# Kernel optimization log

Hardware: AMD Instinct MI355X
Metric: run time of the kernel (lower is better)

Reference implementation:

```python
import jax, jax.numpy as jnp
import numpy as np


def setup_inputs() -> dict:
    key = jax.random.key(0)
    kq, kk, kv = jax.random.split(key, 3)
    B, S, D = 16, 2048, 128
    q = jax.random.normal(kq, (B, S, D), dtype=jnp.float32)
    k = jax.random.normal(kk, (B, S, D), dtype=jnp.float32)
    v = jax.random.normal(kv, (B, S, D), dtype=jnp.float32)
    return {"q": q, "k": k, "v": v}


def reference(q, k, v):
    # q: (B, Sq, Dk), k: (B, Skv, Dk), v: (B, Skv, Dv)
    d_k = k.shape[-1]
    scale = 1.0 / jnp.sqrt(jnp.asarray(d_k, dtype=q.dtype))
    scores = jnp.einsum("bqd,bkd->bqk", q, k) * scale  # (B, Sq, Skv)
    # causal mask: strictly-upper-triangular positions set to -inf (mask=True in init)
    Sq = q.shape[-2]
    causal = jnp.triu(jnp.ones((Sq, Sq), dtype=bool), k=1)
    scores = jnp.where(causal, -jnp.inf, scores)
    attn = jax.nn.softmax(scores, axis=-1)
    return jnp.einsum("bqk,bkd->bqd", attn, v)
```

## Files before the change

kernel.cpp:

```cpp
#include <hip/hip_runtime.h>
#include <hip/hip_bf16.h>

typedef __bf16 bf16;
typedef bf16 bf16x8 __attribute__((ext_vector_type(8)));
typedef bf16 bf16x4 __attribute__((ext_vector_type(4)));
typedef float f32x4 __attribute__((ext_vector_type(4)));

#define DHEAD 128
#define SCL2 0.1275500811965365f
#define NINF (-__builtin_inff())

__device__ __forceinline__ unsigned pk2(float a, float b) {
  bf16 x = (bf16)a, y = (bf16)b;
  unsigned short ux = __builtin_bit_cast(unsigned short, x);
  unsigned short uy = __builtin_bit_cast(unsigned short, y);
  return ((unsigned)uy << 16) | (unsigned)ux;
}

#define ACC_FLOATS (1024 * 64 * 128)
#define ML_OFF ACC_FLOATS
#define WS_NEED ((size_t)(ACC_FLOATS + 1024 * 64 * 2) * 4)

#define ACC4_FLOATS (2048 * 64 * 128)
#define ML4_OFF ACC4_FLOATS
#define WS_NEED4 ((size_t)(ACC4_FLOATS + 2048 * 64 * 2) * 4)

__global__ __launch_bounds__(256) void fa_split4(
    const float* __restrict__ Q, const float* __restrict__ K,
    const float* __restrict__ V, float* __restrict__ ws, int S)
{
  const int bid  = blockIdx.x;
  const int half = bid >> 9;
  const int w    = bid & 511;
  const int qt   = 31 - (w >> 4);
  const int b    = w & 15;
  const int blk  = bid;

  const int NT = 2 * (qt + 1);
  const int t0 = (half * NT) >> 2;
  const int t1 = ((half + 1) * NT) >> 2;

  const int tid  = threadIdx.x;
  const int wave = tid >> 6;
  const int lane = tid & 63;
  const int lr   = lane & 15;
  const int lg   = lane >> 4;

  __shared__ bf16 Ks[32][136];
  __shared__ bf16 Vt[DHEAD][40];
  __shared__ bf16 Ps[4][16][40];

  const size_t bo = (size_t)b * S * DHEAD;
  const float* Qb = Q + bo + (size_t)qt * 64 * DHEAD;
  const float* Kb = K + bo;
  const float* Vb = V + bo;
  const int wrow0 = qt * 64 + wave * 16;

  const int j   = tid & 31;
  const int prw = tid >> 5;
  const int d4  = j << 2;
  const int Gw  = (j >> 1) & 3;

  bf16x8 qf[4];
  {
    const float* qr = Qb + (size_t)(wave * 16 + lr) * DHEAD;
    #pragma unroll
    for (int c = 0; c < 4; ++c) {
      const float4 u0 = *reinterpret_cast<const float4*>(qr + c * 32 + lg * 8);
      const float4 u1 = *reinterpret_cast<const float4*>(qr + c * 32 + lg * 8 + 4);
      bf16x8 f;
      f[0] = (bf16)(u0.x * SCL2); f[1] = (bf16)(u0.y * SCL2);
      f[2] = (bf16)(u0.z * SCL2); f[3] = (bf16)(u0.w * SCL2);
      f[4] = (bf16)(u1.x * SCL2); f[5] = (bf16)(u1.y * SCL2);
      f[6] = (bf16)(u1.z * SCL2); f[7] = (bf16)(u1.w * SCL2);
      qf[c] = f;
    }
  }

  f32x4 oacc[8];
  #pragma unroll
  for (int ii = 0; ii < 8; ++ii) oacc[ii] = (f32x4){0.f, 0.f, 0.f, 0.f};
  float m = NINF, l = 0.f;

  float4 kA[2], kB[2], vA[2], vB[2];
  auto load_tile = [&](int kc) {
    #pragma unroll
    for (int ps = 0; ps < 2; ++ps) {
      const int kv = kc + 2 * (prw + 8 * ps);
      const float* kp = Kb + (size_t)kv * DHEAD + d4;
      const float* vp = Vb + (size_t)kv * DHEAD + d4;
      kA[ps] = *reinterpret_cast<const float4*>(kp);
      kB[ps] = *reinterpret_cast<const float4*>(kp + DHEAD);
      vA[ps] = *reinterpret_cast<const float4*>(vp);
      vB[ps] = *reinterpret_cast<const float4*>(vp + DHEAD);
    }
  };
  auto write_tile = [&]() {
    #pragma unroll
    for (int ps = 0; ps < 2; ++ps) {
      const int kvp = prw + 8 * ps;
      bf16x4 ka, kb;
      ka[0] = (bf16)kA[ps].x; ka[1] = (bf16)kA[ps].y;
      ka[2] = (bf16)kA[ps].z; ka[3] = (bf16)kA[ps].w;
      kb[0] = (bf16)kB[ps].x; kb[1] = (bf16)kB[ps].y;
      kb[2] = (bf16)kB[ps].z; kb[3] = (bf16)kB[ps].w;
      *reinterpret_cast<bf16x4*>(&Ks[2 * kvp][d4])     = ka;
      *reinterpret_cast<bf16x4*>(&Ks[2 * kvp + 1][d4]) = kb;
      const int pS = kvp ^ (Gw << 2);
      const float* fa = &vA[ps].x;
      const float* fb = &vB[ps].x;
      #pragma unroll
      for (int c = 0; c < 4; ++c) {
        *reinterpret_cast<unsigned*>(&Vt[d4 + c][2 * pS]) = pk2(fa[c], fb[c]);
      }
    }
  };

  if (t0 < t1) load_tile(t0 * 32);

  for (int t = t0; t < t1; ++t) {
    __syncthreads();
    write_tile();
    if (t + 1 < t1) load_tile((t + 1) * 32);
    __syncthreads();

    const int kc = t * 32;
    if (kc <= wrow0 + 15) {
      f32x4 s0 = {0.f, 0.f, 0.f, 0.f}, s1 = {0.f, 0.f, 0.f, 0.f};
      __builtin_amdgcn_s_setprio(1);
      #pragma unroll
      for (int c = 0; c < 4; ++c) {
        const bf16x8 kf0 = *reinterpret_cast<const bf16x8*>(&Ks[lr][c * 32 + lg * 8]);
        const bf16x8 kf1 = *reinterpret_cast<const bf16x8*>(&Ks[16 + lr][c * 32 + lg * 8]);
        s0 = __builtin_amdgcn_mfma_f32_16x16x32_bf16(kf0, qf[c], s0, 0, 0, 0);
        s1 = __builtin_amdgcn_mfma_f32_16x16x32_bf16(kf1, qf[c], s1, 0, 0, 0);
      }
      __builtin_amdgcn_s_setprio(0);

      const int qg = wrow0 + lr;
      float x0[4], x1[4];
      if (kc + 31 > wrow0) {
        #pragma unroll
        for (int rr = 0; rr < 4; ++rr) {
          x0[rr] = (kc + 4 * lg + rr      > qg) ? NINF : s0[rr];
          x1[rr] = (kc + 16 + 4 * lg + rr > qg) ? NINF : s1[rr];
        }
      } else {
        #pragma unroll
        for (int rr = 0; rr < 4; ++rr) { x0[rr] = s0[rr]; x1[rr] = s1[rr]; }
      }
      float tm = NINF;
      #pragma unroll
      for (int rr = 0; rr < 4; ++rr) tm = fmaxf(tm, fmaxf(x0[rr], x1[rr]));
      tm = fmaxf(tm, __shfl_xor(tm, 16));
      tm = fmaxf(tm, __shfl_xor(tm, 32));

      if (!__all(tm <= m + 8.0f)) {
        const float mn = fmaxf(m, tm);
        const float al = __builtin_exp2f(m - mn);
        m = mn; l *= al;
        #pragma unroll
        for (int rr = 0; rr < 4; ++rr) {
          const float ar = __shfl(al, 4 * lg + rr);
          #pragma unroll
          for (int ds = 0; ds < 8; ++ds) oacc[ds][rr] *= ar;
        }
      }

      float p0[4], p1[4];
      float ts = 0.f;
      #pragma unroll
      for (int rr = 0; rr < 4; ++rr) {
        p0[rr] = __builtin_exp2f(x0[rr] - m);
        p1[rr] = __builtin_exp2f(x1[rr] - m);
        ts += p0[rr] + p1[rr];
      }
      ts += __shfl_xor(ts, 16);
      ts += __shfl_xor(ts, 32);
      l += ts;

      *reinterpret_cast<unsigned*>(&Ps[wave][lr][4 * lg])          = pk2(p0[0], p0[1]);
      *reinterpret_cast<unsigned*>(&Ps[wave][lr][4 * lg + 2])      = pk2(p0[2], p0[3]);
      *reinterpret_cast<unsigned*>(&Ps[wave][lr][16 + 4 * lg])     = pk2(p1[0], p1[1]);
      *reinterpret_cast<unsigned*>(&Ps[wave][lr][16 + 4 * lg + 2]) = pk2(p1[2], p1[3]);

      const bf16x8 pf = *reinterpret_cast<const bf16x8*>(&Ps[wave][lr][lg * 8]);
      __builtin_amdgcn_s_setprio(1);
      #pragma unroll
      for (int ds = 0; ds < 8; ++ds) {
        const int G = (2 * ds + (lr >> 3)) & 3;
        const bf16x8 vf = *reinterpret_cast<const bf16x8*>(&Vt[ds * 16 + lr][8 * (lg ^ G)]);
        oacc[ds] = __builtin_amdgcn_mfma_f32_16x16x32_bf16(pf, vf, oacc[ds], 0, 0, 0);
      }
      __builtin_amdgcn_s_setprio(0);
    }
  }

  float* aw = ws + (size_t)blk * 8192 + (size_t)(wave * 16) * 128;
  #pragma unroll
  for (int rr = 0; rr < 4; ++rr) {
    #pragma unroll
    for (int ds = 0; ds < 8; ++ds) {
      aw[(4 * lg + rr) * 128 + ds * 16 + lr] = oacc[ds][rr];
    }
  }
  if (lg == 0) {
    float* mlp = ws + ML4_OFF + (size_t)(blk * 64 + wave * 16 + lr) * 2;
    mlp[0] = m;
    mlp[1] = l;
  }
}

__global__ __launch_bounds__(256) void fa_merge4(
    const float* __restrict__ ws, float* __restrict__ O, int S)
{
  const int blk2 = blockIdx.x;
  const int b  = blk2 >> 5;
  const int qt = blk2 & 31;
  const int tid = threadIdx.x;
  const int row = tid >> 2;
  const int c0  = (tid & 3) * 32;

  const int w = (31 - qt) * 16 + b;
  float mi[4], li[4];
  float mm = NINF;
  #pragma unroll
  for (int i = 0; i < 4; ++i) {
    const float* ml = ws + ML4_OFF + (size_t)((i * 512 + w) * 64 + row) * 2;
    mi[i] = ml[0]; li[i] = ml[1];
    mm = fmaxf(mm, mi[i]);
  }
  float a[4], den = 0.f;
  #pragma unroll
  for (int i = 0; i < 4; ++i) { a[i] = __builtin_exp2f(mi[i] - mm); den += a[i] * li[i]; }
  const float inv = 1.0f / den;

  float* out = O + ((size_t)b * S + qt * 64 + row) * DHEAD + c0;
  #pragma unroll
  for (int qd = 0; qd < 8; ++qd) {
    float4 acc = {0.f, 0.f, 0.f, 0.f};
    #pragma unroll
    for (int i = 0; i < 4; ++i) {
      const float* wp = ws + (size_t)(i * 512 + w) * 8192 + (size_t)row * 128 + c0;
      const float4 u = *reinterpret_cast<const float4*>(wp + qd * 4);
      acc.x += a[i] * u.x; acc.y += a[i] * u.y;
      acc.z += a[i] * u.z; acc.w += a[i] * u.w;
    }
    float4 o;
    o.x = acc.x * inv; o.y = acc.y * inv; o.z = acc.z * inv; o.w = acc.w * inv;
    *reinterpret_cast<float4*>(out + qd * 4) = o;
  }
}

__global__ __launch_bounds__(256) void fa_split(
    const float* __restrict__ Q, const float* __restrict__ K,
    const float* __restrict__ V, float* __restrict__ ws, int S)
{
  const int bid  = blockIdx.x;
  const int r    = bid >> 8;
  const int i    = bid & 255;
  const int b    = i & 15;
  const int idx  = i >> 4;
  const int qt   = (r < 2) ? (31 - idx) : idx;
  const int half = r & 1;
  const int blk  = bid;

  const int t0 = half * (qt + 1);
  const int t1 = t0 + (qt + 1);

  const int tid  = threadIdx.x;
  const int wave = tid >> 6;
  const int lane = tid & 63;
  const int lr   = lane & 15;
  const int lg   = lane >> 4;

  __shared__ bf16 Ks[2][32][136];
  __shared__ bf16 Vt[2][DHEAD][40];
  __shared__ bf16 Ps[4][16][40];

  const size_t bo = (size_t)b * S * DHEAD;
  const float* Qb = Q + bo + (size_t)qt * 64 * DHEAD;
  const float* Kb = K + bo;
  const float* Vb = V + bo;
  const int wrow0 = qt * 64 + wave * 16;

  const int j   = tid & 31;
  const int prw = tid >> 5;
  const int d4  = j << 2;
  const int Gw  = (j >> 1) & 3;

  bf16x8 qf[4];
  {
    const float* qr = Qb + (size_t)(wave * 16 + lr) * DHEAD;
    #pragma unroll
    for (int c = 0; c < 4; ++c) {
      const float4 u0 = *reinterpret_cast<const float4*>(qr + c * 32 + lg * 8);
      const float4 u1 = *reinterpret_cast<const float4*>(qr + c * 32 + lg * 8 + 4);
      bf16x8 f;
      f[0] = (bf16)u0.x; f[1] = (bf16)u0.y; f[2] = (bf16)u0.z; f[3] = (bf16)u0.w;
      f[4] = (bf16)u1.x; f[5] = (bf16)u1.y; f[6] = (bf16)u1.z; f[7] = (bf16)u1.w;
      qf[c] = f;
    }
  }

  f32x4 oacc[8];
  #pragma unroll
  for (int ii = 0; ii < 8; ++ii) oacc[ii] = (f32x4){0.f, 0.f, 0.f, 0.f};
  float m = NINF, l = 0.f;

  float4 kA[2], kB[2], vA[2], vB[2];
  auto load_tile = [&](int kc) {
    #pragma unroll
    for (int ps = 0; ps < 2; ++ps) {
      const int kv = kc + 2 * (prw + 8 * ps);
      const float* kp = Kb + (size_t)kv * DHEAD + d4;
      const float* vp = Vb + (size_t)kv * DHEAD + d4;
      kA[ps] = *reinterpret_cast<const float4*>(kp);
      kB[ps] = *reinterpret_cast<const float4*>(kp + DHEAD);
      vA[ps] = *reinterpret_cast<const float4*>(vp);
      vB[ps] = *reinterpret_cast<const float4*>(vp + DHEAD);
    }
  };
  auto write_tile = [&](int buf) {
    #pragma unroll
    for (int ps = 0; ps < 2; ++ps) {
      const int kvp = prw + 8 * ps;
      bf16x4 ka, kb;
      ka[0] = (bf16)kA[ps].x; ka[1] = (bf16)kA[ps].y;
      ka[2] = (bf16)kA[ps].z; ka[3] = (bf16)kA[ps].w;
      kb[0] = (bf16)kB[ps].x; kb[1] = (bf16)kB[ps].y;
      kb[2] = (bf16)kB[ps].z; kb[3] = (bf16)kB[ps].w;
      *reinterpret_cast<bf16x4*>(&Ks[buf][2 * kvp][d4])     = ka;
      *reinterpret_cast<bf16x4*>(&Ks[buf][2 * kvp + 1][d4]) = kb;
      const int pS = kvp ^ (Gw << 2);
      const float* fa = &vA[ps].x;
      const float* fb = &vB[ps].x;
      #pragma unroll
      for (int c = 0; c < 4; ++c) {
        *reinterpret_cast<unsigned*>(&Vt[buf][d4 + c][2 * pS]) = pk2(fa[c], fb[c]);
      }
    }
  };

  load_tile(t0 * 32);
  write_tile(0);
  if (t0 + 1 < t1) load_tile((t0 + 1) * 32);

  int cur = 0;
  for (int t = t0; t < t1; ++t) {
    __syncthreads();
    if (t + 1 < t1) write_tile(cur ^ 1);
    if (t + 2 < t1) load_tile((t + 2) * 32);

    const int kc = t * 32;
    if (kc <= wrow0 + 15) {
      f32x4 s0 = {0.f, 0.f, 0.f, 0.f}, s1 = {0.f, 0.f, 0.f, 0.f};
      __builtin_amdgcn_s_setprio(1);
      #pragma unroll
      for (int c = 0; c < 4; ++c) {
        const bf16x8 kf0 = *reinterpret_cast<const bf16x8*>(&Ks[cur][lr][c * 32 + lg * 8]);
        const bf16x8 kf1 = *reinterpret_cast<const bf16x8*>(&Ks[cur][16 + lr][c * 32 + lg * 8]);
        s0 = __builtin_amdgcn_mfma_f32_16x16x32_bf16(kf0, qf[c], s0, 0, 0, 0);
        s1 = __builtin_amdgcn_mfma_f32_16x16x32_bf16(kf1, qf[c], s1, 0, 0, 0);
      }
      __builtin_amdgcn_s_setprio(0);

      const int qg = wrow0 + lr;
      float x0[4], x1[4];
      if (kc + 31 > wrow0) {
        #pragma unroll
        for (int rr = 0; rr < 4; ++rr) {
          x0[rr] = (kc + 4 * lg + rr      > qg) ? NINF : s0[rr] * SCL2;
          x1[rr] = (kc + 16 + 4 * lg + rr > qg) ? NINF : s1[rr] * SCL2;
        }
      } else {
        #pragma unroll
        for (int rr = 0; rr < 4; ++rr) { x0[rr] = s0[rr] * SCL2; x1[rr] = s1[rr] * SCL2; }
      }
      float tm = NINF;
      #pragma unroll
      for (int rr = 0; rr < 4; ++rr) tm = fmaxf(tm, fmaxf(x0[rr], x1[rr]));
      tm = fmaxf(tm, __shfl_xor(tm, 16));
      tm = fmaxf(tm, __shfl_xor(tm, 32));

      if (!__all(tm <= m + 8.0f)) {
        const float mn = fmaxf(m, tm);
        const float al = __builtin_exp2f(m - mn);
        m = mn; l *= al;
        #pragma unroll
        for (int rr = 0; rr < 4; ++rr) {
          const float ar = __shfl(al, 4 * lg + rr);
          #pragma unroll
          for (int ds = 0; ds < 8; ++ds) oacc[ds][rr] *= ar;
        }
      }

      float p0[4], p1[4];
      float ts = 0.f;
      #pragma unroll
      for (int rr = 0; rr < 4; ++rr) {
        p0[rr] = __builtin_exp2f(x0[rr] - m);
        p1[rr] = __builtin_exp2f(x1[rr] - m);
        ts += p0[rr] + p1[rr];
      }
      ts += __shfl_xor(ts, 16);
      ts += __shfl_xor(ts, 32);
      l += ts;

      *reinterpret_cast<unsigned*>(&Ps[wave][lr][4 * lg])          = pk2(p0[0], p0[1]);
      *reinterpret_cast<unsigned*>(&Ps[wave][lr][4 * lg + 2])      = pk2(p0[2], p0[3]);
      *reinterpret_cast<unsigned*>(&Ps[wave][lr][16 + 4 * lg])     = pk2(p1[0], p1[1]);
      *reinterpret_cast<unsigned*>(&Ps[wave][lr][16 + 4 * lg + 2]) = pk2(p1[2], p1[3]);

      const bf16x8 pf = *reinterpret_cast<const bf16x8*>(&Ps[wave][lr][lg * 8]);
      __builtin_amdgcn_s_setprio(1);
      #pragma unroll
      for (int ds = 0; ds < 8; ++ds) {
        const int G = (2 * ds + (lr >> 3)) & 3;
        const bf16x8 vf = *reinterpret_cast<const bf16x8*>(&Vt[cur][ds * 16 + lr][8 * (lg ^ G)]);
        oacc[ds] = __builtin_amdgcn_mfma_f32_16x16x32_bf16(pf, vf, oacc[ds], 0, 0, 0);
      }
      __builtin_amdgcn_s_setprio(0);
    }
    cur ^= 1;
  }

  float* aw = ws + (size_t)blk * 8192 + (size_t)(wave * 16) * 128;
  #pragma unroll
  for (int rr = 0; rr < 4; ++rr) {
    #pragma unroll
    for (int ds = 0; ds < 8; ++ds) {
      aw[(4 * lg + rr) * 128 + ds * 16 + lr] = oacc[ds][rr];
    }
  }
  if (lg == 0) {
    float* mlp = ws + ML_OFF + (size_t)(blk * 64 + wave * 16 + lr) * 2;
    mlp[0] = m;
    mlp[1] = l;
  }
}

__global__ __launch_bounds__(256) void fa_merge(
    const float* __restrict__ ws, float* __restrict__ O, int S)
{
  const int blk2 = blockIdx.x;
  const int b  = blk2 >> 5;
  const int qt = blk2 & 31;
  const int tid = threadIdx.x;
  const int row = tid >> 2;
  const int c0  = (tid & 3) * 32;

  const int idx  = (qt >= 16) ? (31 - qt) : qt;
  const int base = (qt >= 16) ? 0 : 512;
  const int blk0 = base + (idx << 4) + b;
  const int blk1 = blk0 + 256;

  const float* ml0 = ws + ML_OFF + (size_t)(blk0 * 64 + row) * 2;
  const float* ml1 = ws + ML_OFF + (size_t)(blk1 * 64 + row) * 2;
  const float m0 = ml0[0], l0 = ml0[1];
  const float m1 = ml1[0], l1 = ml1[1];
  const float mm = fmaxf(m0, m1);
  const float a0 = __builtin_exp2f(m0 - mm);
  const float a1 = __builtin_exp2f(m1 - mm);
  const float inv = 1.0f / (a0 * l0 + a1 * l1);

  const float* w0 = ws + (size_t)blk0 * 8192 + (size_t)row * 128 + c0;
  const float* w1 = ws + (size_t)blk1 * 8192 + (size_t)row * 128 + c0;
  float* out = O + ((size_t)b * S + qt * 64 + row) * DHEAD + c0;

  #pragma unroll
  for (int qd = 0; qd < 8; ++qd) {
    const float4 u0 = *reinterpret_cast<const float4*>(w0 + qd * 4);
    const float4 u1 = *reinterpret_cast<const float4*>(w1 + qd * 4);
    float4 o;
    o.x = (a0 * u0.x + a1 * u1.x) * inv;
    o.y = (a0 * u0.y + a1 * u1.y) * inv;
    o.z = (a0 * u0.z + a1 * u1.z) * inv;
    o.w = (a0 * u0.w + a1 * u1.w) * inv;
    *reinterpret_cast<float4*>(out + qd * 4) = o;
  }
}

__global__ __launch_bounds__(256) void fa_fwd(
    const float* __restrict__ Q, const float* __restrict__ K,
    const float* __restrict__ V, float* __restrict__ O, int S)
{
  const int bid = blockIdx.x;
  const int prb = bid & 255;
  const int hb  = bid >> 8;
  const int b   = prb & 15;
  const int jj  = prb >> 4;
  const int qt  = hb ? jj : (31 - jj);

  const int tid  = threadIdx.x;
  const int wave = tid >> 6;
  const int lane = tid & 63;
  const int lr   = lane & 15;
  const int lg   = lane >> 4;

  __shared__ bf16 Ks[2][32][136];
  __shared__ bf16 Vt[2][DHEAD][40];
  __shared__ bf16 Ps[4][16][40];

  const size_t bo = (size_t)b * S * DHEAD;
  const float* Qb = Q + bo + (size_t)qt * 64 * DHEAD;
  const float* Kb = K + bo;
  const float* Vb = V + bo;
  const int wrow0 = qt * 64 + wave * 16;

  const int j   = tid & 31;
  const int prw = tid >> 5;
  const int d4  = j << 2;
  const int Gw  = (j >> 1) & 3;

  bf16x8 qf[4];
  {
    const float* qr = Qb + (size_t)(wave * 16 + lr) * DHEAD;
    #pragma unroll
    for (int c = 0; c < 4; ++c) {
      const float4 u0 = *reinterpret_cast<const float4*>(qr + c * 32 + lg * 8);
      const float4 u1 = *reinterpret_cast<const float4*>(qr + c * 32 + lg * 8 + 4);
      bf16x8 f;
      f[0] = (bf16)u0.x; f[1] = (bf16)u0.y; f[2] = (bf16)u0.z; f[3] = (bf16)u0.w;
      f[4] = (bf16)u1.x; f[5] = (bf16)u1.y; f[6] = (bf16)u1.z; f[7] = (bf16)u1.w;
      qf[c] = f;
    }
  }

  f32x4 oacc[8];
  #pragma unroll
  for (int ii = 0; ii < 8; ++ii) oacc[ii] = (f32x4){0.f, 0.f, 0.f, 0.f};
  float m = NINF, l = 0.f;

  const int nt = 2 * (qt + 1);
  float4 kA[2], kB[2], vA[2], vB[2];

  auto load_tile = [&](int kc) {
    #pragma unroll
    for (int ps = 0; ps < 2; ++ps) {
      const int kv = kc + 2 * (prw + 8 * ps);
      const float* kp = Kb + (size_t)kv * DHEAD + d4;
      const float* vp = Vb + (size_t)kv * DHEAD + d4;
      kA[ps] = *reinterpret_cast<const float4*>(kp);
      kB[ps] = *reinterpret_cast<const float4*>(kp + DHEAD);
      vA[ps] = *reinterpret_cast<const float4*>(vp);
      vB[ps] = *reinterpret_cast<const float4*>(vp + DHEAD);
    }
  };
  auto write_tile = [&](int buf) {
    #pragma unroll
    for (int ps = 0; ps < 2; ++ps) {
      const int kvp = prw + 8 * ps;
      bf16x4 ka, kb;
      ka[0] = (bf16)kA[ps].x; ka[1] = (bf16)kA[ps].y;
      ka[2] = (bf16)kA[ps].z; ka[3] = (bf16)kA[ps].w;
      kb[0] = (bf16)kB[ps].x; kb[1] = (bf16)kB[ps].y;
      kb[2] = (bf16)kB[ps].z; kb[3] = (bf16)kB[ps].w;
      *reinterpret_cast<bf16x4*>(&Ks[buf][2 * kvp][d4])     = ka;
      *reinterpret_cast<bf16x4*>(&Ks[buf][2 * kvp + 1][d4]) = kb;
      const int pS = kvp ^ (Gw << 2);
      const float* fa = &vA[ps].x;
      const float* fb = &vB[ps].x;
      #pragma unroll
      for (int c = 0; c < 4; ++c) {
        *reinterpret_cast<unsigned*>(&Vt[buf][d4 + c][2 * pS]) = pk2(fa[c], fb[c]);
      }
    }
  };

  load_tile(0);
  write_tile(0);
  if (nt > 1) load_tile(32);

  int cur = 0;
  for (int t = 0; t < nt; ++t) {
    __syncthreads();
    if (t + 1 < nt) write_tile(cur ^ 1);
    if (t + 2 < nt) load_tile((t + 2) * 32);

    const int kc = t * 32;
    if (kc <= wrow0 + 15) {
      f32x4 s0 = {0.f, 0.f, 0.f, 0.f}, s1 = {0.f, 0.f, 0.f, 0.f};
      __builtin_amdgcn_s_setprio(1);
      #pragma unroll
      for (int c = 0; c < 4; ++c) {
        const bf16x8 kf0 = *reinterpret_cast<const bf16x8*>(&Ks[cur][lr][c * 32 + lg * 8]);
        const bf16x8 kf1 = *reinterpret_cast<const bf16x8*>(&Ks[cur][16 + lr][c * 32 + lg * 8]);
        s0 = __builtin_amdgcn_mfma_f32_16x16x32_bf16(kf0, qf[c], s0, 0, 0, 0);
        s1 = __builtin_amdgcn_mfma_f32_16x16x32_bf16(kf1, qf[c], s1, 0, 0, 0);
      }
      __builtin_amdgcn_s_setprio(0);

      const int qg = wrow0 + lr;
      float x0[4], x1[4];
      if (kc + 31 > wrow0) {
        #pragma unroll
        for (int rr = 0; rr < 4; ++rr) {
          x0[rr] = (kc + 4 * lg + rr      > qg) ? NINF : s0[rr] * SCL2;
          x1[rr] = (kc + 16 + 4 * lg + rr > qg) ? NINF : s1[rr] * SCL2;
        }
      } else {
        #pragma unroll
        for (int rr = 0; rr < 4; ++rr) { x0[rr] = s0[rr] * SCL2; x1[rr] = s1[rr] * SCL2; }
      }
      float tm = NINF;
      #pragma unroll
      for (int rr = 0; rr < 4; ++rr) tm = fmaxf(tm, fmaxf(x0[rr], x1[rr]));
      tm = fmaxf(tm, __shfl_xor(tm, 16));
      tm = fmaxf(tm, __shfl_xor(tm, 32));

      if (!__all(tm <= m + 8.0f)) {
        const float mn = fmaxf(m, tm);
        const float al = __builtin_exp2f(m - mn);
        m = mn; l *= al;
        #pragma unroll
        for (int rr = 0; rr < 4; ++rr) {
          const float ar = __shfl(al, 4 * lg + rr);
          #pragma unroll
          for (int ds = 0; ds < 8; ++ds) oacc[ds][rr] *= ar;
        }
      }

      float p0[4], p1[4];
      float ts = 0.f;
      #pragma unroll
      for (int rr = 0; rr < 4; ++rr) {
        p0[rr] = __builtin_exp2f(x0[rr] - m);
        p1[rr] = __builtin_exp2f(x1[rr] - m);
        ts += p0[rr] + p1[rr];
      }
      ts += __shfl_xor(ts, 16);
      ts += __shfl_xor(ts, 32);
      l += ts;

      *reinterpret_cast<unsigned*>(&Ps[wave][lr][4 * lg])          = pk2(p0[0], p0[1]);
      *reinterpret_cast<unsigned*>(&Ps[wave][lr][4 * lg + 2])      = pk2(p0[2], p0[3]);
      *reinterpret_cast<unsigned*>(&Ps[wave][lr][16 + 4 * lg])     = pk2(p1[0], p1[1]);
      *reinterpret_cast<unsigned*>(&Ps[wave][lr][16 + 4 * lg + 2]) = pk2(p1[2], p1[3]);

      const bf16x8 pf = *reinterpret_cast<const bf16x8*>(&Ps[wave][lr][lg * 8]);
      __builtin_amdgcn_s_setprio(1);
      #pragma unroll
      for (int ds = 0; ds < 8; ++ds) {
        const int G = (2 * ds + (lr >> 3)) & 3;
        const bf16x8 vf = *reinterpret_cast<const bf16x8*>(&Vt[cur][ds * 16 + lr][8 * (lg ^ G)]);
        oacc[ds] = __builtin_amdgcn_mfma_f32_16x16x32_bf16(pf, vf, oacc[ds], 0, 0, 0);
      }
      __builtin_amdgcn_s_setprio(0);
    }
    cur ^= 1;
  }

  const float linv = 1.0f / l;
  float* Ob = O + bo + (size_t)(qt * 64 + wave * 16) * DHEAD;
  #pragma unroll
  for (int rr = 0; rr < 4; ++rr) {
    const float ir = __shfl(linv, 4 * lg + rr);
    #pragma unroll
    for (int ds = 0; ds < 8; ++ds) {
      Ob[(size_t)(4 * lg + rr) * DHEAD + ds * 16 + lr] = oacc[ds][rr] * ir;
    }
  }
}

extern "C" void kernel_launch(void* const* d_in, const int* in_sizes, int n_in,
                              void* d_out, int out_size, void* d_ws, size_t ws_size,
                              hipStream_t stream) {
  const float* q = (const float*)d_in[0];
  const float* k = (const float*)d_in[1];
  const float* v = (const float*)d_in[2];
  float* o = (float*)d_out;

  const int B = 16;
  const int S = in_sizes[0] / (B * DHEAD);

  if (ws_size >= WS_NEED4 && S == 2048) {
    float* ws = (float*)d_ws;
    fa_split4<<<dim3(2048), dim3(256), 0, stream>>>(q, k, v, ws, S);
    fa_merge4<<<dim3(512), dim3(256), 0, stream>>>(ws, o, S);
  } else if (ws_size >= WS_NEED && S == 2048) {
    float* ws = (float*)d_ws;
    fa_split<<<dim3(1024), dim3(256), 0, stream>>>(q, k, v, ws, S);
    fa_merge<<<dim3(512), dim3(256), 0, stream>>>(ws, o, S);
  } else {
    fa_fwd<<<dim3(512), dim3(256), 0, stream>>>(q, k, v, o, S);
  }
}
```

Baseline: 185.4 us.

## Pre-convert K/V to bf16 with transposed V and read MFMA operands from global

Adds a prep kernel that converts K to bf16 and V to a bf16 transposed layout in workspace. The new split kernel then reads MFMA operands straight from global/L2 instead of staging them through LDS with double buffering and barriers. Q is prescaled before the bf16 cast, and the block order is remapped for L2 locality, with a matching merge kernel. This removes repeated fp32 K/V loads and conversions per query tile and drops the syncthreads, but adds an extra launch and global traffic, and relies on cache hits for the uncoalesced-ish direct loads. The fallback paths are kept and the old two-way split path is removed.

Measured after the change: 257.6 us. 1.39x slower.

```diff
diff --git a/kernel.cpp b/kernel.cpp
--- a/kernel.cpp
+++ b/kernel.cpp
@@ -17,13 +17,239 @@
   return ((unsigned)uy << 16) | (unsigned)ux;
 }
 
-#define ACC_FLOATS (1024 * 64 * 128)
-#define ML_OFF ACC_FLOATS
-#define WS_NEED ((size_t)(ACC_FLOATS + 1024 * 64 * 2) * 4)
-
 #define ACC4_FLOATS (2048 * 64 * 128)
 #define ML4_OFF ACC4_FLOATS
-#define WS_NEED4 ((size_t)(ACC4_FLOATS + 2048 * 64 * 2) * 4)
+#define ACC_ML_FLOATS (ACC4_FLOATS + 2048 * 64 * 2)
+#define WS_NEED4 ((size_t)ACC_ML_FLOATS * 4)
+#define KV_BASE_BYTES ((size_t)ACC_ML_FLOATS * 4)
+#define KV_BYTES ((size_t)16 * 2048 * 128 * 2)
+#define WS_DIRECT (KV_BASE_BYTES + 2 * KV_BYTES)
+
+__global__ __launch_bounds__(256) void fa_prep(
+    const float* __restrict__ K, const float* __restrict__ V,
+    bf16* __restrict__ Kb, bf16* __restrict__ Vt, int S)
+{
+  const int b   = blockIdx.x >> 5;
+  const int kv0 = (blockIdx.x & 31) * 64;
+  const int tid = threadIdx.x;
+
+  __shared__ float Vl[64][132];
+
+  const float* Kbase = K + ((size_t)b * S + kv0) * DHEAD;
+  const float* Vbase = V + ((size_t)b * S + kv0) * DHEAD;
+  bf16* Kout = Kb + ((size_t)b * S + kv0) * DHEAD;
+
+  #pragma unroll
+  for (int i = 0; i < 8; ++i) {
+    const int flat = i * 256 + tid;
+    const int row  = flat >> 5;
+    const int c4   = (flat & 31) << 2;
+    const float4 kv4 = *reinterpret_cast<const float4*>(Kbase + (size_t)row * DHEAD + c4);
+    bf16x4 kp;
+    kp[0] = (bf16)kv4.x; kp[1] = (bf16)kv4.y; kp[2] = (bf16)kv4.z; kp[3] = (bf16)kv4.w;
+    *reinterpret_cast<bf16x4*>(Kout + (size_t)row * DHEAD + c4) = kp;
+    const float4 vv4 = *reinterpret_cast<const float4*>(Vbase + (size_t)row * DHEAD + c4);
+    Vl[row][c4 + 0] = vv4.x; Vl[row][c4 + 1] = vv4.y;
+    Vl[row][c4 + 2] = vv4.z; Vl[row][c4 + 3] = vv4.w;
+  }
+  __syncthreads();
+
+  #pragma unroll
+  for (int i = 0; i < 8; ++i) {
+    const int flat = i * 256 + tid;
+    const int d    = flat >> 4;
+    const int kvg  = (flat & 15) << 2;
+    bf16x4 vp;
+    vp[0] = (bf16)Vl[kvg + 0][d]; vp[1] = (bf16)Vl[kvg + 1][d];
+    vp[2] = (bf16)Vl[kvg + 2][d]; vp[3] = (bf16)Vl[kvg + 3][d];
+    *reinterpret_cast<bf16x4*>(Vt + ((size_t)b * DHEAD + d) * S + kv0 + kvg) = vp;
+  }
+}
+
+__global__ __launch_bounds__(256) void fa_direct(
+    const float* __restrict__ Q, const bf16* __restrict__ Kb,
+    const bf16* __restrict__ Vt, float* __restrict__ ws, int S)
+{
+  const int bid  = blockIdx.x;
+  const int blo  = bid & 7;
+  const int rest = bid >> 3;
+  const int half = rest & 3;
+  const int bhi  = (rest >> 2) & 1;
+  const int qt   = 31 - (rest >> 3);
+  const int b    = blo | (bhi << 3);
+  const int blk  = bid;
+
+  const int NT = 2 * (qt + 1);
+  const int t0 = (half * NT) >> 2;
+  const int t1 = ((half + 1) * NT) >> 2;
+
+  const int tid  = threadIdx.x;
+  const int wave = tid >> 6;
+  const int lane = tid & 63;
+  const int lr   = lane & 15;
+  const int lg   = lane >> 4;
+
+  __shared__ bf16 Ps[4][16][40];
+
+  const float* Qb = Q + ((size_t)b * S + qt * 64) * DHEAD;
+  const bf16* Kbb = Kb + (size_t)b * S * DHEAD;
+  const bf16* Vtb = Vt + (size_t)b * DHEAD * S;
+  const int wrow0 = qt * 64 + wave * 16;
+
+  bf16x8 qf[4];
+  {
+    const float* qr = Qb + (size_t)(wave * 16 + lr) * DHEAD;
+    #pragma unroll
+    for (int c = 0; c < 4; ++c) {
+      const float4 u0 = *reinterpret_cast<const float4*>(qr + c * 32 + lg * 8);
+      const float4 u1 = *reinterpret_cast<const float4*>(qr + c * 32 + lg * 8 + 4);
+      bf16x8 f;
+      f[0] = (bf16)(u0.x * SCL2); f[1] = (bf16)(u0.y * SCL2);
+      f[2] = (bf16)(u0.z * SCL2); f[3] = (bf16)(u0.w * SCL2);
+      f[4] = (bf16)(u1.x * SCL2); f[5] = (bf16)(u1.y * SCL2);
+      f[6] = (bf16)(u1.z * SCL2); f[7] = (bf16)(u1.w * SCL2);
+      qf[c] = f;
+    }
+  }
+
+  f32x4 oacc[8];
+  #pragma unroll
+  for (int ii = 0; ii < 8; ++ii) oacc[ii] = (f32x4){0.f, 0.f, 0.f, 0.f};
+  float m = NINF, l = 0.f;
+
+  for (int t = t0; t < t1; ++t) {
+    const int kc = t * 32;
+    if (kc > wrow0 + 15) continue;
+
+    const bf16* krow0 = Kbb + (size_t)(kc + lr) * DHEAD + lg * 8;
+    const bf16* krow1 = krow0 + 16 * DHEAD;
+    f32x4 s0 = {0.f, 0.f, 0.f, 0.f}, s1 = {0.f, 0.f, 0.f, 0.f};
+    __builtin_amdgcn_s_setprio(1);
+    #pragma unroll
+    for (int c = 0; c < 4; ++c) {
+      const bf16x8 kf0 = *reinterpret_cast<const bf16x8*>(krow0 + c * 32);
+      const bf16x8 kf1 = *reinterpret_cast<const bf16x8*>(krow1 + c * 32);
+      s0 = __builtin_amdgcn_mfma_f32_16x16x32_bf16(kf0, qf[c], s0, 0, 0, 0);
+      s1 = __builtin_amdgcn_mfma_f32_16x16x32_bf16(kf1, qf[c], s1, 0, 0, 0);
+    }
+    __builtin_amdgcn_s_setprio(0);
+
+    const int qg = wrow0 + lr;
+    float x0[4], x1[4];
+    if (kc + 31 > wrow0) {
+      #pragma unroll
+      for (int rr = 0; rr < 4; ++rr) {
+        x0[rr] = (kc + 4 * lg + rr      > qg) ? NINF : s0[rr];
+        x1[rr] = (kc + 16 + 4 * lg + rr > qg) ? NINF : s1[rr];
+      }
+    } else {
+      #pragma unroll
+      for (int rr = 0; rr < 4; ++rr) { x0[rr] = s0[rr]; x1[rr] = s1[rr]; }
+    }
+    float tm = NINF;
+    #pragma unroll
+    for (int rr = 0; rr < 4; ++rr) tm = fmaxf(tm, fmaxf(x0[rr], x1[rr]));
+    tm = fmaxf(tm, __shfl_xor(tm, 16));
+    tm = fmaxf(tm, __shfl_xor(tm, 32));
+
+    if (!__all(tm <= m + 8.0f)) {
+      const float mn = fmaxf(m, tm);
+      const float al = __builtin_exp2f(m - mn);
+      m = mn; l *= al;
+      #pragma unroll
+      for (int rr = 0; rr < 4; ++rr) {
+        const float ar = __shfl(al, 4 * lg + rr);
+        #pragma unroll
+        for (int ds = 0; ds < 8; ++ds) oacc[ds][rr] *= ar;
+      }
+    }
+
+    float p0[4], p1[4];
+    float ts = 0.f;
+    #pragma unroll
+    for (int rr = 0; rr < 4; ++rr) {
+      p0[rr] = __builtin_exp2f(x0[rr] - m);
+      p1[rr] = __builtin_exp2f(x1[rr] - m);
+      ts += p0[rr] + p1[rr];
+    }
+    ts += __shfl_xor(ts, 16);
+    ts += __shfl_xor(ts, 32);
+    l += ts;
+
+    *reinterpret_cast<unsigned*>(&Ps[wave][lr][4 * lg])          = pk2(p0[0], p0[1]);
+    *reinterpret_cast<unsigned*>(&Ps[wave][lr][4 * lg + 2])      = pk2(p0[2], p0[3]);
+    *reinterpret_cast<unsigned*>(&Ps[wave][lr][16 + 4 * lg])     = pk2(p1[0], p1[1]);
+    *reinterpret_cast<unsigned*>(&Ps[wave][lr][16 + 4 * lg + 2]) = pk2(p1[2], p1[3]);
+
+    const bf16x8 pf = *reinterpret_cast<const bf16x8*>(&Ps[wave][lr][lg * 8]);
+
+    const bf16* vrow = Vtb + (size_t)lr * S + kc + lg * 8;
+    __builtin_amdgcn_s_setprio(1);
+    #pragma unroll
+    for (int ds = 0; ds < 8; ++ds) {
+      const bf16x8 vf = *reinterpret_cast<const bf16x8*>(vrow + (size_t)(ds * 16) * S);
+      oacc[ds] = __builtin_amdgcn_mfma_f32_16x16x32_bf16(pf, vf, oacc[ds], 0, 0, 0);
+    }
+    __builtin_amdgcn_s_setprio(0);
+  }
+
+  float* aw = ws + (size_t)blk * 8192 + (size_t)(wave * 16) * 128;
+  #pragma unroll
+  for (int rr = 0; rr < 4; ++rr) {
+    #pragma unroll
+    for (int ds = 0; ds < 8; ++ds) {
+      aw[(4 * lg + rr) * 128 + ds * 16 + lr] = oacc[ds][rr];
+    }
+  }
+  if (lg == 0) {
+    float* mlp = ws + ML4_OFF + (size_t)(blk * 64 + wave * 16 + lr) * 2;
+    mlp[0] = m;
+    mlp[1] = l;
+  }
+}
+
+__global__ __launch_bounds__(256) void fa_merge4d(
+    const float* __restrict__ ws, float* __restrict__ O, int S)
+{
+  const int blk2 = blockIdx.x;
+  const int b  = blk2 >> 5;
+  const int qt = blk2 & 31;
+  const int tid = threadIdx.x;
+  const int row = tid >> 2;
+  const int c0  = (tid & 3) * 32;
+
+  const int blo = b & 7, bhi = b >> 3;
+  float mi[4], li[4];
+  float mm = NINF;
+  int blks[4];
+  #pragma unroll
+  for (int i = 0; i < 4; ++i) {
+    blks[i] = ((((31 - qt) << 3) | (bhi << 2) | i) << 3) | blo;
+    const float* ml = ws + ML4_OFF + (size_t)(blks[i] * 64 + row) * 2;
+    mi[i] = ml[0]; li[i] = ml[1];
+    mm = fmaxf(mm, mi[i]);
+  }
+  float a[4], den = 0.f;
+  #pragma unroll
+  for (int i = 0; i < 4; ++i) { a[i] = __builtin_exp2f(mi[i] - mm); den += a[i] * li[i]; }
+  const float inv = 1.0f / den;
+
+  float* out = O + ((size_t)b * S + qt * 64 + row) * DHEAD + c0;
+  #pragma unroll
+  for (int qd = 0; qd < 8; ++qd) {
+    float4 acc = {0.f, 0.f, 0.f, 0.f};
+    #pragma unroll
+    for (int i = 0; i < 4; ++i) {
+      const float* wp = ws + (size_t)blks[i] * 8192 + (size_t)row * 128 + c0;
+      const float4 u = *reinterpret_cast<const float4*>(wp + qd * 4);
+      acc.x += a[i] * u.x; acc.y += a[i] * u.y;
+      acc.z += a[i] * u.z; acc.w += a[i] * u.w;
+    }
+    float4 o;
+    o.x = acc.x * inv; o.y = acc.y * inv; o.z = acc.z * inv; o.w = acc.w * inv;
+    *reinterpret_cast<float4*>(out + qd * 4) = o;
+  }
+}
 
 __global__ __launch_bounds__(256) void fa_split4(
     const float* __restrict__ Q, const float* __restrict__ K,
@@ -252,21 +478,16 @@
   }
 }
 
-__global__ __launch_bounds__(256) void fa_split(
+__global__ __launch_bounds__(256) void fa_fwd(
     const float* __restrict__ Q, const float* __restrict__ K,
-    const float* __restrict__ V, float* __restrict__ ws, int S)
+    const float* __restrict__ V, float* __restrict__ O, int S)
 {
-  const int bid  = blockIdx.x;
-  const int r    = bid >> 8;
-  const int i    = bid & 255;
-  const int b    = i & 15;
-  const int idx  = i >> 4;
-  const int qt   = (r < 2) ? (31 - idx) : idx;
-  const int half = r & 1;
-  const int blk  = bid;
-
-  const int t0 = half * (qt + 1);
-  const int t1 = t0 + (qt + 1);
+  const int bid = blockIdx.x;
+  const int prb = bid & 255;
+  const int hb  = bid >> 8;
+  const int b   = prb & 15;
+  const int jj  = prb >> 4;
+  const int qt  = hb ? jj : (31 - jj);
 
   const int tid  = threadIdx.x;
   const int wave = tid >> 6;
@@ -308,7 +529,9 @@
   for (int ii = 0; ii < 8; ++ii) oacc[ii] = (f32x4){0.f, 0.f, 0.f, 0.f};
   float m = NINF, l = 0.f;
 
+  const int nt = 2 * (qt + 1);
   float4 kA[2], kB[2], vA[2], vB[2];
+
   auto load_tile = [&](int kc) {
     #pragma unroll
     for (int ps = 0; ps < 2; ++ps) {
@@ -342,15 +565,15 @@
     }
   };
 
-  load_tile(t0 * 32);
+  load_tile(0);
   write_tile(0);
-  if (t0 + 1 < t1) load_tile((t0 + 1) * 32);
+  if (nt > 1) load_tile(32);
 
   int cur = 0;
-  for (int t = t0; t < t1; ++t) {
+  for (int t = 0; t < nt; ++t) {
     __syncthreads();
-    if (t + 1 < t1) write_tile(cur ^ 1);
-    if (t + 2 < t1) load_tile((t + 2) * 32);
+    if (t + 1 < nt) write_tile(cur ^ 1);
+    if (t + 2 < nt) load_tile((t + 2) * 32);
 
     const int kc = t * 32;
     if (kc <= wrow0 + 15) {
@@ -425,232 +648,6 @@
     cur ^= 1;
   }
 
-  float* aw = ws + (size_t)blk * 8192 + (size_t)(wave * 16) * 128;
-  #pragma unroll
-  for (int rr = 0; rr < 4; ++rr) {
-    #pragma unroll
-    for (int ds = 0; ds < 8; ++ds) {
-      aw[(4 * lg + rr) * 128 + ds * 16 + lr] = oacc[ds][rr];
-    }
-  }
-  if (lg == 0) {
-    float* mlp = ws + ML_OFF + (size_t)(blk * 64 + wave * 16 + lr) * 2;
-    mlp[0] = m;
-    mlp[1] = l;
-  }
-}
-
-__global__ __launch_bounds__(256) void fa_merge(
-    const float* __restrict__ ws, float* __restrict__ O, int S)
-{
-  const int blk2 = blockIdx.x;
-  const int b  = blk2 >> 5;
-  const int qt = blk2 & 31;
-  const int tid = threadIdx.x;
-  const int row = tid >> 2;
-  const int c0  = (tid & 3) * 32;
-
-  const int idx  = (qt >= 16) ? (31 - qt) : qt;
-  const int base = (qt >= 16) ? 0 : 512;
-  const int blk0 = base + (idx << 4) + b;
-  const int blk1 = blk0 + 256;
-
-  const float* ml0 = ws + ML_OFF + (size_t)(blk0 * 64 + row) * 2;
-  const float* ml1 = ws + ML_OFF + (size_t)(blk1 * 64 + row) * 2;
-  const float m0 = ml0[0], l0 = ml0[1];
-  const float m1 = ml1[0], l1 = ml1[1];
-  const float mm = fmaxf(m0, m1);
-  const float a0 = __builtin_exp2f(m0 - mm);
-  const float a1 = __builtin_exp2f(m1 - mm);
-  const float inv = 1.0f / (a0 * l0 + a1 * l1);
-
-  const float* w0 = ws + (size_t)blk0 * 8192 + (size_t)row * 128 + c0;
-  const float* w1 = ws + (size_t)blk1 * 8192 + (size_t)row * 128 + c0;
-  float* out = O + ((size_t)b * S + qt * 64 + row) * DHEAD + c0;
-
-  #pragma unroll
-  for (int qd = 0; qd < 8; ++qd) {
-    const float4 u0 = *reinterpret_cast<const float4*>(w0 + qd * 4);
-    const float4 u1 = *reinterpret_cast<const float4*>(w1 + qd * 4);
-    float4 o;
-    o.x = (a0 * u0.x + a1 * u1.x) * inv;
-    o.y = (a0 * u0.y + a1 * u1.y) * inv;
-    o.z = (a0 * u0.z + a1 * u1.z) * inv;
-    o.w = (a0 * u0.w + a1 * u1.w) * inv;
-    *reinterpret_cast<float4*>(out + qd * 4) = o;
-  }
-}
-
-__global__ __launch_bounds__(256) void fa_fwd(
-    const float* __restrict__ Q, const float* __restrict__ K,
-    const float* __restrict__ V, float* __restrict__ O, int S)
-{
-  const int bid = blockIdx.x;
-  const int prb = bid & 255;
-  const int hb  = bid >> 8;
-  const int b   = prb & 15;
-  const int jj  = prb >> 4;
-  const int qt  = hb ? jj : (31 - jj);
-
-  const int tid  = threadIdx.x;
-  const int wave = tid >> 6;
-  const int lane = tid & 63;
-  const int lr   = lane & 15;
-  const int lg   = lane >> 4;
-
-  __shared__ bf16 Ks[2][32][136];
-  __shared__ bf16 Vt[2][DHEAD][40];
-  __shared__ bf16 Ps[4][16][40];
-
-  const size_t bo = (size_t)b * S * DHEAD;
-  const float* Qb = Q + bo + (size_t)qt * 64 * DHEAD;
-  const float* Kb = K + bo;
-  const float* Vb = V + bo;
-  const int wrow0 = qt * 64 + wave * 16;
-
-  const int j   = tid & 31;
-  const int prw = tid >> 5;
-  const int d4  = j << 2;
-  const int Gw  = (j >> 1) & 3;
-
-  bf16x8 qf[4];
-  {
-    const float* qr = Qb + (size_t)(wave * 16 + lr) * DHEAD;
-    #pragma unroll
-    for (int c = 0; c < 4; ++c) {
-      const float4 u0 = *reinterpret_cast<const float4*>(qr + c * 32 + lg * 8);
-      const float4 u1 = *reinterpret_cast<const float4*>(qr + c * 32 + lg * 8 + 4);
-      bf16x8 f;
-      f[0] = (bf16)u0.x; f[1] = (bf16)u0.y; f[2] = (bf16)u0.z; f[3] = (bf16)u0.w;
-      f[4] = (bf16)u1.x; f[5] = (bf16)u1.y; f[6] = (bf16)u1.z; f[7] = (bf16)u1.w;
-      qf[c] = f;
-    }
-  }
-
-  f32x4 oacc[8];
-  #pragma unroll
-  for (int ii = 0; ii < 8; ++ii) oacc[ii] = (f32x4){0.f, 0.f, 0.f, 0.f};
-  float m = NINF, l = 0.f;
-
-  const int nt = 2 * (qt + 1);
-  float4 kA[2], kB[2], vA[2], vB[2];
-
-  auto load_tile = [&](int kc) {
-    #pragma unroll
-    for (int ps = 0; ps < 2; ++ps) {
-      const int kv = kc + 2 * (prw + 8 * ps);
-      const float* kp = Kb + (size_t)kv * DHEAD + d4;
-      const float* vp = Vb + (size_t)kv * DHEAD + d4;
-      kA[ps] = *reinterpret_cast<const float4*>(kp);
-      kB[ps] = *reinterpret_cast<const float4*>(kp + DHEAD);
-      vA[ps] = *reinterpret_cast<const float4*>(vp);
-      vB[ps] = *reinterpret_cast<const float4*>(vp + DHEAD);
-    }
-  };
-  auto write_tile = [&](int buf) {
-    #pragma unroll
-    for (int ps = 0; ps < 2; ++ps) {
-      const int kvp = prw + 8 * ps;
-      bf16x4 ka, kb;
-      ka[0] = (bf16)kA[ps].x; ka[1] = (bf16)kA[ps].y;
-      ka[2] = (bf16)kA[ps].z; ka[3] = (bf16)kA[ps].w;
-      kb[0] = (bf16)kB[ps].x; kb[1] = (bf16)kB[ps].y;
-      kb[2] = (bf16)kB[ps].z; kb[3] = (bf16)kB[ps].w;
-      *reinterpret_cast<bf16x4*>(&Ks[buf][2 * kvp][d4])     = ka;
-      *reinterpret_cast<bf16x4*>(&Ks[buf][2 * kvp + 1][d4]) = kb;
-      const int pS = kvp ^ (Gw << 2);
-      const float* fa = &vA[ps].x;
-      const float* fb = &vB[ps].x;
-      #pragma unroll
-      for (int c = 0; c < 4; ++c) {
-        *reinterpret_cast<unsigned*>(&Vt[buf][d4 + c][2 * pS]) = pk2(fa[c], fb[c]);
-      }
-    }
-  };
-
-  load_tile(0);
-  write_tile(0);
-  if (nt > 1) load_tile(32);
-
-  int cur = 0;
-  for (int t = 0; t < nt; ++t) {
-    __syncthreads();
-    if (t + 1 < nt) write_tile(cur ^ 1);
-    if (t + 2 < nt) load_tile((t + 2) * 32);
-
-    const int kc = t * 32;
-    if (kc <= wrow0 + 15) {
-      f32x4 s0 = {0.f, 0.f, 0.f, 0.f}, s1 = {0.f, 0.f, 0.f, 0.f};
-      __builtin_amdgcn_s_setprio(1);
-      #pragma unroll
-      for (int c = 0; c < 4; ++c) {
-        const bf16x8 kf0 = *reinterpret_cast<const bf16x8*>(&Ks[cur][lr][c * 32 + lg * 8]);
-        const bf16x8 kf1 = *reinterpret_cast<const bf16x8*>(&Ks[cur][16 + lr][c * 32 + lg * 8]);
-        s0 = __builtin_amdgcn_mfma_f32_16x16x32_bf16(kf0, qf[c], s0, 0, 0, 0);
-        s1 = __builtin_amdgcn_mfma_f32_16x16x32_bf16(kf1, qf[c], s1, 0, 0, 0);
-      }
-      __builtin_amdgcn_s_setprio(0);
-
-      const int qg = wrow0 + lr;
-      float x0[4], x1[4];
-      if (kc + 31 > wrow0) {
-        #pragma unroll
-        for (int rr = 0; rr < 4; ++rr) {
-          x0[rr] = (kc + 4 * lg + rr      > qg) ? NINF : s0[rr] * SCL2;
-          x1[rr] = (kc + 16 + 4 * lg + rr > qg) ? NINF : s1[rr] * SCL2;
-        }
-      } else {
-        #pragma unroll
-        for (int rr = 0; rr < 4; ++rr) { x0[rr] = s0[rr] * SCL2; x1[rr] = s1[rr] * SCL2; }
-      }
-      float tm = NINF;
-      #pragma unroll
-      for (int rr = 0; rr < 4; ++rr) tm = fmaxf(tm, fmaxf(x0[rr], x1[rr]));
-      tm = fmaxf(tm, __shfl_xor(tm, 16));
-      tm = fmaxf(tm, __shfl_xor(tm, 32));
-
-      if (!__all(tm <= m + 8.0f)) {
-        const float mn = fmaxf(m, tm);
-        const float al = __builtin_exp2f(m - mn);
-        m = mn; l *= al;
-        #pragma unroll
-        for (int rr = 0; rr < 4; ++rr) {
-          const float ar = __shfl(al, 4 * lg + rr);
-          #pragma unroll
-          for (int ds = 0; ds < 8; ++ds) oacc[ds][rr] *= ar;
-        }
-      }
-
-      float p0[4], p1[4];
-      float ts = 0.f;
-      #pragma unroll
-      for (int rr = 0; rr < 4; ++rr) {
-        p0[rr] = __builtin_exp2f(x0[rr] - m);
-        p1[rr] = __builtin_exp2f(x1[rr] - m);
-        ts += p0[rr] + p1[rr];
-      }
-      ts += __shfl_xor(ts, 16);
-      ts += __shfl_xor(ts, 32);
-      l += ts;
-
-      *reinterpret_cast<unsigned*>(&Ps[wave][lr][4 * lg])          = pk2(p0[0], p0[1]);
-      *reinterpret_cast<unsigned*>(&Ps[wave][lr][4 * lg + 2])      = pk2(p0[2], p0[3]);
-      *reinterpret_cast<unsigned*>(&Ps[wave][lr][16 + 4 * lg])     = pk2(p1[0], p1[1]);
-      *reinterpret_cast<unsigned*>(&Ps[wave][lr][16 + 4 * lg + 2]) = pk2(p1[2], p1[3]);
-
-      const bf16x8 pf = *reinterpret_cast<const bf16x8*>(&Ps[wave][lr][lg * 8]);
-      __builtin_amdgcn_s_setprio(1);
-      #pragma unroll
-      for (int ds = 0; ds < 8; ++ds) {
-        const int G = (2 * ds + (lr >> 3)) & 3;
-        const bf16x8 vf = *reinterpret_cast<const bf16x8*>(&Vt[cur][ds * 16 + lr][8 * (lg ^ G)]);
-        oacc[ds] = __builtin_amdgcn_mfma_f32_16x16x32_bf16(pf, vf, oacc[ds], 0, 0, 0);
-      }
-      __builtin_amdgcn_s_setprio(0);
-    }
-    cur ^= 1;
-  }
-
   const float linv = 1.0f / l;
   float* Ob = O + bo + (size_t)(qt * 64 + wave * 16) * DHEAD;
   #pragma unroll
@@ -674,14 +671,17 @@
   const int B = 16;
   const int S = in_sizes[0] / (B * DHEAD);
 
-  if (ws_size >= WS_NEED4 && S == 2048) {
+  if (ws_size >= WS_DIRECT && S == 2048) {
+    float* ws = (float*)d_ws;
+    bf16* kb = (bf16*)((char*)d_ws + KV_BASE_BYTES);
+    bf16* vt = (bf16*)((char*)d_ws + KV_BASE_BYTES + KV_BYTES);
+    fa_prep<<<dim3(512), dim3(256), 0, stream>>>(k, v, kb, vt, S);
+    fa_direct<<<dim3(2048), dim3(256), 0, stream>>>(q, kb, vt, ws, S);
+    fa_merge4d<<<dim3(512), dim3(256), 0, stream>>>(ws, o, S);
+  } else if (ws_size >= WS_NEED4 && S == 2048) {
     float* ws = (float*)d_ws;
     fa_split4<<<dim3(2048), dim3(256), 0, stream>>>(q, k, v, ws, S);
     fa_merge4<<<dim3(512), dim3(256), 0, stream>>>(ws, o, S);
-  } else if (ws_size >= WS_NEED && S == 2048) {
-    float* ws = (float*)d_ws;
-    fa_split<<<dim3(1024), dim3(256), 0, stream>>>(q, k, v, ws, S);
-    fa_merge<<<dim3(512), dim3(256), 0, stream>>>(ws, o, S);
   } else {
     fa_fwd<<<dim3(512), dim3(256), 0, stream>>>(q, k, v, o, S);
   }
```
